# Kernel tuning notes

Measured on AMD Instinct MI355X. Metric: run time of the kernel, lower is better.

Reference implementation:

```python
import jax, jax.numpy as jnp
import numpy as np

N_ITER = 5  # Newton-Schulz iterations (matches n_iter default in source)


def _isqrt_newton_schulz_batch(A, num_iters):
    # A: [B, C, C] SPD matrices -> A^{-1/2} via coupled Newton-Schulz,
    # exactly mirroring isqrt_newton_schulz_autograd_batch in the source.
    b, dim, _ = A.shape
    normA = jnp.sqrt(jnp.sum(A * A, axis=(1, 2), keepdims=True))  # Frobenius norm per batch
    Y = A / normA
    I = jnp.broadcast_to(jnp.eye(dim, dtype=A.dtype), A.shape)
    Z = I
    for _ in range(num_iters):
        T = 0.5 * (3.0 * I - Z @ Y)
        Y = Y @ T
        Z = T @ Z
    return Z / jnp.sqrt(normA)


def setup_inputs() -> dict:
    key = jax.random.key(0)
    k1, k2, k3 = jax.random.split(key, 3)
    B, C, H, W = 8, 256, 128, 128
    r = 8  # reduction
    x = jax.random.normal(k1, (B, C, H, W), dtype=jnp.float32)
    w1 = jax.random.normal(k2, (C // r, C), dtype=jnp.float32) * 0.05  # squeeze 1x1 conv
    b1 = jnp.zeros((C // r,), dtype=jnp.float32)
    w2 = jax.random.normal(k3, (C, C // r), dtype=jnp.float32) * 0.05  # excite 1x1 conv
    b2 = jnp.zeros((C,), dtype=jnp.float32)
    return {"x": x, "w1": w1, "b1": b1, "w2": w2, "b2": b2}


def reference(x, w1, b1, w2, b2):
    B, C, H, W = x.shape
    M = H * W
    # global second-order (covariance) pooling
    xf = x.reshape(B, C, M)
    xc = xf - jnp.mean(xf, axis=-1, keepdims=True)          # center over spatial dim
    cov = jnp.einsum('bcm,bdm->bcd', xc, xc) / M            # [B, C, C]
    A_isqrt = _isqrt_newton_schulz_batch(cov, N_ITER)       # [B, C, C]
    # channel statistic: row mean of the matrix-(inverse-)sqrt
    y = jnp.mean(A_isqrt, axis=-1)                          # [B, C]
    # squeeze-excite gating (1x1 convs == dense over channels)
    h = jax.nn.relu(y @ w1.T + b1)                          # [B, C//r]
    g = jax.nn.sigmoid(h @ w2.T + b2)                       # [B, C]
    return x * g[:, :, None, None]
```

## Files before the change

### kernel.cpp

```cpp
#include <hip/hip_runtime.h>
#include <cstdint>
#include <cstddef>

typedef short s8vec __attribute__((ext_vector_type(8)));
typedef float f16acc __attribute__((ext_vector_type(16)));

#define C_DIM 256
#define M_DIM 16384
#define BATCH 8
#define KSPLIT 32
#define KCHUNK 512
#define BK 64
#define LDSP 72

static __device__ __forceinline__ unsigned short f2bf(float f) {
    union { float f; unsigned u; } v; v.f = f;
    unsigned r = v.u + 0x7fffu + ((v.u >> 16) & 1u);
    return (unsigned short)(r >> 16);
}
static __device__ __forceinline__ float bf2f(unsigned short h) {
    union { unsigned u; float f; } v; v.u = ((unsigned)h) << 16;
    return v.f;
}

__global__ __launch_bounds__(1024, 1)
void cov_kernel(const float* __restrict__ x, float* __restrict__ covraw,
                float* __restrict__ sums)
{
    __shared__ unsigned short Xs[C_DIM][LDSP];
    const int b   = blockIdx.y;
    const int kc  = blockIdx.x;
    const int tid = threadIdx.x;
    const int lane = tid & 63;
    const int wave = tid >> 6;
    const int wr = wave >> 2;
    const int wc = wave & 3;
    const int half = lane >> 5;
    const int l31  = lane & 31;

    const float* xb = x + (size_t)b * C_DIM * M_DIM + (size_t)kc * KCHUNK;

    f16acc acc[2][2] = {};
    float rowsum[4] = {0, 0, 0, 0};
    const int r0 = tid >> 4;
    const int c0 = (tid & 15) * 4;

    float4 v[4];
    {
        const float* src = xb + (size_t)r0 * M_DIM + c0;
        #pragma unroll
        for (int i = 0; i < 4; ++i)
            v[i] = *(const float4*)(src + (size_t)(64 * i) * M_DIM);
    }

    for (int kt = 0; kt < KCHUNK / BK; ++kt) {
        __syncthreads();
        #pragma unroll
        for (int i = 0; i < 4; ++i) {
            rowsum[i] += v[i].x + v[i].y + v[i].z + v[i].w;
            ushort4 p;
            p.x = f2bf(v[i].x); p.y = f2bf(v[i].y);
            p.z = f2bf(v[i].z); p.w = f2bf(v[i].w);
            *(ushort4*)&Xs[r0 + 64 * i][c0] = p;
        }
        if (kt < KCHUNK / BK - 1) {
            const float* src = xb + (size_t)r0 * M_DIM + (kt + 1) * BK + c0;
            #pragma unroll
            for (int i = 0; i < 4; ++i)
                v[i] = *(const float4*)(src + (size_t)(64 * i) * M_DIM);
        }
        __syncthreads();
        #pragma unroll
        for (int ks = 0; ks < 4; ++ks) {
            const int k0 = ks * 16 + half * 8;
            s8vec af[2], bfr[2];
            #pragma unroll
            for (int i = 0; i < 2; ++i)
                af[i] = *(const s8vec*)&Xs[wr * 64 + i * 32 + l31][k0];
            #pragma unroll
            for (int j = 0; j < 2; ++j)
                bfr[j] = *(const s8vec*)&Xs[wc * 64 + j * 32 + l31][k0];
            #pragma unroll
            for (int i = 0; i < 2; ++i)
                #pragma unroll
                for (int j = 0; j < 2; ++j)
                    acc[i][j] = __builtin_amdgcn_mfma_f32_32x32x16_bf16(
                        af[i], bfr[j], acc[i][j], 0, 0, 0);
        }
    }
    #pragma unroll
    for (int i = 0; i < 4; ++i) {
        float s = rowsum[i];
        s += __shfl_down(s, 8, 16);
        s += __shfl_down(s, 4, 16);
        s += __shfl_down(s, 2, 16);
        s += __shfl_down(s, 1, 16);
        if ((lane & 15) == 0)
            atomicAdd(&sums[b * C_DIM + r0 + 64 * i], s);
    }
    float* covb = covraw + (size_t)b * C_DIM * C_DIM;
    #pragma unroll
    for (int i = 0; i < 2; ++i) {
        const int rb = wr * 64 + i * 32 + 4 * half;
        #pragma unroll
        for (int j = 0; j < 2; ++j) {
            const int cb = wc * 64 + j * 32 + l31;
            #pragma unroll
            for (int r = 0; r < 16; ++r) {
                const int row = rb + (r & 3) + 8 * (r >> 2);
                atomicAdd(&covb[row * C_DIM + cb], acc[i][j][r]);
            }
        }
    }
}

__global__ __launch_bounds__(1024)
void finalize_cov(const float* __restrict__ covraw, const float* __restrict__ sums,
                  float* __restrict__ normA_g, unsigned short* __restrict__ Y0,
                  unsigned short* __restrict__ T0)
{
    const int b = blockIdx.x;
    const int tid = threadIdx.x;
    const float invM = 1.0f / (float)M_DIM;
    const float* cb = covraw + (size_t)b * 65536;
    const float* sb = sums + b * 256;
    float ss = 0.0f;
    #pragma unroll 4
    for (int i = 0; i < 64; ++i) {
        const int e = tid + i * 1024;
        const int r = e >> 8, c = e & 255;
        float v = cb[e] * invM - (sb[r] * invM) * (sb[c] * invM);
        ss += v * v;
    }
    __shared__ float red[16];
    __shared__ float sh_inv;
    float s = ss;
    #pragma unroll
    for (int off = 32; off; off >>= 1) s += __shfl_down(s, off, 64);
    if ((tid & 63) == 0) red[tid >> 6] = s;
    __syncthreads();
    if (tid == 0) {
        float t = 0.0f;
        #pragma unroll
        for (int i = 0; i < 16; ++i) t += red[i];
        float na = sqrtf(t);
        normA_g[b] = na;
        sh_inv = 1.0f / na;
    }
    __syncthreads();
    const float inv = sh_inv;
    unsigned short* yb = Y0 + (size_t)b * 65536;
    unsigned short* tb = T0 + (size_t)b * 65536;
    #pragma unroll 4
    for (int i = 0; i < 64; ++i) {
        const int e = tid + i * 1024;
        const int r = e >> 8, c = e & 255;
        float v = (cb[e] * invM - (sb[r] * invM) * (sb[c] * invM)) * inv;
        yb[e] = f2bf(v);
        tb[e] = f2bf(((r == c) ? 1.5f : 0.0f) - 0.5f * v);
    }
}

__global__ __launch_bounds__(256, 4)
void ns_stage(const unsigned short* __restrict__ A0, const unsigned short* __restrict__ B0,
              unsigned short* __restrict__ C0,
              const unsigned short* __restrict__ A1, const unsigned short* __restrict__ B1,
              unsigned short* __restrict__ C1,
              float c0, float c1)
{
    __shared__ unsigned short As[64][LDSP];
    __shared__ unsigned short Bs[64][LDSP];
    const int b = blockIdx.y;
    const int trow = (blockIdx.x >> 2) * 64, tcol = (blockIdx.x & 3) * 64;
    const unsigned short* A = (blockIdx.z ? A1 : A0) + (size_t)b * 65536;
    const unsigned short* B = (blockIdx.z ? B1 : B0) + (size_t)b * 65536;
    unsigned short* Cp = (blockIdx.z ? C1 : C0) + (size_t)b * 65536;

    const int tid = threadIdx.x;
    const int lane = tid & 63, wave = tid >> 6;
    const int wr = wave >> 1, wc = wave & 1;
    const int half = lane >> 5, l31 = lane & 31;

    f16acc acc = {};

    const int sr = tid >> 3;
    const int sc = (tid & 7) * 8;
    for (int kt = 0; kt < 4; ++kt) {
        const int kb = kt * BK;
        uint4 va[2], vb[2];
        #pragma unroll
        for (int i = 0; i < 2; ++i) {
            va[i] = *(const uint4*)(A + (size_t)(trow + sr + 32 * i) * 256 + kb + sc);
            vb[i] = *(const uint4*)(B + (size_t)(tcol + sr + 32 * i) * 256 + kb + sc);
        }
        __syncthreads();
        #pragma unroll
        for (int i = 0; i < 2; ++i) {
            *(uint4*)&As[sr + 32 * i][sc] = va[i];
            *(uint4*)&Bs[sr + 32 * i][sc] = vb[i];
        }
        __syncthreads();
        #pragma unroll
        for (int ks = 0; ks < 4; ++ks) {
            const int k0 = ks * 16 + half * 8;
            s8vec af = *(const s8vec*)&As[wr * 32 + l31][k0];
            s8vec bfr = *(const s8vec*)&Bs[wc * 32 + l31][k0];
            acc = __builtin_amdgcn_mfma_f32_32x32x16_bf16(af, bfr, acc, 0, 0, 0);
        }
    }
    const int rb = trow + wr * 32 + 4 * half;
    const int cb = tcol + wc * 32 + l31;
    #pragma unroll
    for (int r = 0; r < 16; ++r) {
        const int row = rb + (r & 3) + 8 * (r >> 2);
        float v = c1 * acc[r] + ((row == cb) ? c0 : 0.0f);
        Cp[row * 256 + cb] = f2bf(v);
    }
}

__global__ __launch_bounds__(256)
void gating_kernel(const unsigned short* __restrict__ Zfin, const float* __restrict__ normA_g,
                   const float* __restrict__ w1, const float* __restrict__ b1,
                   const float* __restrict__ w2, const float* __restrict__ b2,
                   float* __restrict__ g)
{
    const int b = blockIdx.x;
    const int tid = threadIdx.x;
    __shared__ float sy[256];
    __shared__ float sh[32];
    const unsigned short* zr = Zfin + (size_t)b * 65536 + (size_t)tid * 256;
    float s = 0.0f;
    #pragma unroll
    for (int i = 0; i < 32; ++i) {
        uint4 v = *(const uint4*)(zr + i * 8);
        const unsigned short* p = (const unsigned short*)&v;
        #pragma unroll
        for (int j = 0; j < 8; ++j) s += bf2f(p[j]);
    }
    const float scale = (1.0f / 256.0f) / sqrtf(normA_g[b]);
    sy[tid] = s * scale;
    __syncthreads();
    if (tid < 32) {
        float hh = b1[tid];
        const float* w1r = w1 + tid * 256;
        for (int c = 0; c < 256; ++c) hh += w1r[c] * sy[c];
        sh[tid] = hh > 0.0f ? hh : 0.0f;
    }
    __syncthreads();
    float z = b2[tid];
    const float* w2r = w2 + tid * 32;
    #pragma unroll
    for (int j = 0; j < 32; ++j) z += w2r[j] * sh[j];
    g[b * 256 + tid] = 1.0f / (1.0f + expf(-z));
}

__global__ __launch_bounds__(256)
void scale_kernel(const float* __restrict__ x, const float* __restrict__ g,
                  float* __restrict__ out)
{
    const float4* x4 = (const float4*)x;
    float4* o4 = (float4*)out;
    #pragma unroll
    for (int it = 0; it < 4; ++it) {
        size_t i = (size_t)blockIdx.x * 1024 + it * 256 + threadIdx.x;
        float gg = g[i >> 12];
        float4 v = x4[i];
        float4 r;
        r.x = v.x * gg; r.y = v.y * gg; r.z = v.z * gg; r.w = v.w * gg;
        o4[i] = r;
    }
}

extern "C" void kernel_launch(void* const* d_in, const int* in_sizes, int n_in,
                              void* d_out, int out_size, void* d_ws, size_t ws_size,
                              hipStream_t stream)
{
    const float* x  = (const float*)d_in[0];
    const float* w1 = (const float*)d_in[1];
    const float* b1 = (const float*)d_in[2];
    const float* w2 = (const float*)d_in[3];
    const float* b2 = (const float*)d_in[4];
    float* out = (float*)d_out;

    char* ws = (char*)d_ws;
    float* covraw = (float*)ws;
    float* sums   = (float*)(ws + 2097152);
    float* normA  = (float*)(ws + 2105344);
    float* g      = (float*)(ws + 2106368);
    unsigned short* Ya = (unsigned short*)(ws + 4194304);
    unsigned short* Yb = (unsigned short*)(ws + 5242880);
    unsigned short* Za = (unsigned short*)(ws + 6291456);
    unsigned short* Zb = (unsigned short*)(ws + 7340032);
    unsigned short* T  = (unsigned short*)(ws + 8388608);

    hipMemsetAsync(covraw, 0, 2105344, stream);

    cov_kernel<<<dim3(KSPLIT, BATCH), 1024, 0, stream>>>(x, covraw, sums);
    finalize_cov<<<BATCH, 1024, 0, stream>>>(covraw, sums, normA, Ya, Za);

    ns_stage<<<dim3(16, BATCH, 1), 256, 0, stream>>>(Ya, Za, Yb, Ya, Za, Yb, 0.0f, 1.0f);

    unsigned short* Ycur = Yb; unsigned short* Yoth = Ya;
    unsigned short* Zcur = Za; unsigned short* Zoth = Zb;
    for (int it = 0; it < 4; ++it) {
        ns_stage<<<dim3(16, BATCH, 1), 256, 0, stream>>>(
            Zcur, Ycur, T, Zcur, Ycur, T, 1.5f, -0.5f);
        if (it < 3) {
            ns_stage<<<dim3(16, BATCH, 2), 256, 0, stream>>>(
                Ycur, T, Yoth, T, Zcur, Zoth, 0.0f, 1.0f);
            unsigned short* t0 = Ycur; Ycur = Yoth; Yoth = t0;
            unsigned short* t1 = Zcur; Zcur = Zoth; Zoth = t1;
        } else {
            ns_stage<<<dim3(16, BATCH, 1), 256, 0, stream>>>(
                T, Zcur, Zoth, T, Zcur, Zoth, 0.0f, 1.0f);
            Zcur = Zoth;
        }
    }
    gating_kernel<<<BATCH, 256, 0, stream>>>(Zcur, normA, w1, b1, w2, b2, g);
    scale_kernel<<<8192, 256, 0, stream>>>(x, g, out);
}
```

Measured before the change: 447.7 us.

## Exploit covariance symmetry in split-K cov kernel and parallelize finalize

```diff
diff --git a/kernel.cpp b/kernel.cpp
--- a/kernel.cpp
+++ b/kernel.cpp
@@ -23,51 +23,78 @@
     return v.f;
 }
 
-__global__ __launch_bounds__(1024, 1)
+__global__ __launch_bounds__(256, 2)
 void cov_kernel(const float* __restrict__ x, float* __restrict__ covraw,
                 float* __restrict__ sums)
 {
-    __shared__ unsigned short Xs[C_DIM][LDSP];
-    const int b   = blockIdx.y;
-    const int kc  = blockIdx.x;
-    const int tid = threadIdx.x;
+    __shared__ unsigned short As[128][LDSP];
+    __shared__ unsigned short Bs[128][LDSP];
+    const int tile = blockIdx.x;
+    const int kc   = blockIdx.y;
+    const int b    = blockIdx.z;
+    const int trow = (tile == 0) ? 0 : 128;
+    const int tcol = (tile == 2) ? 0 : trow;
+    const bool diag = (tile < 2);
+
+    const int tid  = threadIdx.x;
     const int lane = tid & 63;
     const int wave = tid >> 6;
-    const int wr = wave >> 2;
-    const int wc = wave & 3;
-    const int half = lane >> 5;
-    const int l31  = lane & 31;
+    const int wr = wave >> 1, wc = wave & 1;
+    const int half = lane >> 5, l31 = lane & 31;
 
     const float* xb = x + (size_t)b * C_DIM * M_DIM + (size_t)kc * KCHUNK;
 
     f16acc acc[2][2] = {};
-    float rowsum[4] = {0, 0, 0, 0};
-    const int r0 = tid >> 4;
-    const int c0 = (tid & 15) * 4;
-
-    float4 v[4];
+    float rowsum[8] = {0,0,0,0,0,0,0,0};
+    const int sr = tid >> 4;
+    const int sc = (tid & 15) * 4;
+
+    float4 va[8], vb[8];
     {
-        const float* src = xb + (size_t)r0 * M_DIM + c0;
-        #pragma unroll
-        for (int i = 0; i < 4; ++i)
-            v[i] = *(const float4*)(src + (size_t)(64 * i) * M_DIM);
-    }
+        const float* sa = xb + (size_t)(trow + sr) * M_DIM + sc;
+        #pragma unroll
+        for (int i = 0; i < 8; ++i)
+            va[i] = *(const float4*)(sa + (size_t)(16 * i) * M_DIM);
+        if (!diag) {
+            const float* sb2 = xb + (size_t)(tcol + sr) * M_DIM + sc;
+            #pragma unroll
+            for (int i = 0; i < 8; ++i)
+                vb[i] = *(const float4*)(sb2 + (size_t)(16 * i) * M_DIM);
+        }
+    }
+
+    const unsigned short (*Bp)[LDSP] = diag ? As : Bs;
 
     for (int kt = 0; kt < KCHUNK / BK; ++kt) {
         __syncthreads();
         #pragma unroll
-        for (int i = 0; i < 4; ++i) {
-            rowsum[i] += v[i].x + v[i].y + v[i].z + v[i].w;
+        for (int i = 0; i < 8; ++i) {
+            if (diag) rowsum[i] += va[i].x + va[i].y + va[i].z + va[i].w;
             ushort4 p;
-            p.x = f2bf(v[i].x); p.y = f2bf(v[i].y);
-            p.z = f2bf(v[i].z); p.w = f2bf(v[i].w);
-            *(ushort4*)&Xs[r0 + 64 * i][c0] = p;
+            p.x = f2bf(va[i].x); p.y = f2bf(va[i].y);
+            p.z = f2bf(va[i].z); p.w = f2bf(va[i].w);
+            *(ushort4*)&As[sr + 16 * i][sc] = p;
+        }
+        if (!diag) {
+            #pragma unroll
+            for (int i = 0; i < 8; ++i) {
+                ushort4 p;
+                p.x = f2bf(vb[i].x); p.y = f2bf(vb[i].y);
+                p.z = f2bf(vb[i].z); p.w = f2bf(vb[i].w);
+                *(ushort4*)&Bs[sr + 16 * i][sc] = p;
+            }
         }
         if (kt < KCHUNK / BK - 1) {
-            const float* src = xb + (size_t)r0 * M_DIM + (kt + 1) * BK + c0;
-            #pragma unroll
-            for (int i = 0; i < 4; ++i)
-                v[i] = *(const float4*)(src + (size_t)(64 * i) * M_DIM);
+            const float* sa = xb + (size_t)(trow + sr) * M_DIM + (kt + 1) * BK + sc;
+            #pragma unroll
+            for (int i = 0; i < 8; ++i)
+                va[i] = *(const float4*)(sa + (size_t)(16 * i) * M_DIM);
+            if (!diag) {
+                const float* sb2 = xb + (size_t)(tcol + sr) * M_DIM + (kt + 1) * BK + sc;
+                #pragma unroll
+                for (int i = 0; i < 8; ++i)
+                    vb[i] = *(const float4*)(sb2 + (size_t)(16 * i) * M_DIM);
+            }
         }
         __syncthreads();
         #pragma unroll
@@ -76,10 +103,10 @@
             s8vec af[2], bfr[2];
             #pragma unroll
             for (int i = 0; i < 2; ++i)
-                af[i] = *(const s8vec*)&Xs[wr * 64 + i * 32 + l31][k0];
+                af[i] = *(const s8vec*)&As[wr * 64 + i * 32 + l31][k0];
             #pragma unroll
             for (int j = 0; j < 2; ++j)
-                bfr[j] = *(const s8vec*)&Xs[wc * 64 + j * 32 + l31][k0];
+                bfr[j] = *(const s8vec*)&Bp[wc * 64 + j * 32 + l31][k0];
             #pragma unroll
             for (int i = 0; i < 2; ++i)
                 #pragma unroll
@@ -88,23 +115,25 @@
                         af[i], bfr[j], acc[i][j], 0, 0, 0);
         }
     }
-    #pragma unroll
-    for (int i = 0; i < 4; ++i) {
-        float s = rowsum[i];
-        s += __shfl_down(s, 8, 16);
-        s += __shfl_down(s, 4, 16);
-        s += __shfl_down(s, 2, 16);
-        s += __shfl_down(s, 1, 16);
-        if ((lane & 15) == 0)
-            atomicAdd(&sums[b * C_DIM + r0 + 64 * i], s);
+    if (diag) {
+        #pragma unroll
+        for (int i = 0; i < 8; ++i) {
+            float s = rowsum[i];
+            s += __shfl_down(s, 8, 16);
+            s += __shfl_down(s, 4, 16);
+            s += __shfl_down(s, 2, 16);
+            s += __shfl_down(s, 1, 16);
+            if ((lane & 15) == 0)
+                atomicAdd(&sums[b * C_DIM + trow + sr + 16 * i], s);
+        }
     }
     float* covb = covraw + (size_t)b * C_DIM * C_DIM;
     #pragma unroll
     for (int i = 0; i < 2; ++i) {
-        const int rb = wr * 64 + i * 32 + 4 * half;
+        const int rb = trow + wr * 64 + i * 32 + 4 * half;
         #pragma unroll
         for (int j = 0; j < 2; ++j) {
-            const int cb = wc * 64 + j * 32 + l31;
+            const int cb = tcol + wc * 64 + j * 32 + l31;
             #pragma unroll
             for (int r = 0; r < 16; ++r) {
                 const int row = rb + (r & 3) + 8 * (r >> 2);
@@ -114,48 +143,56 @@
     }
 }
 
-__global__ __launch_bounds__(1024)
-void finalize_cov(const float* __restrict__ covraw, const float* __restrict__ sums,
-                  float* __restrict__ normA_g, unsigned short* __restrict__ Y0,
-                  unsigned short* __restrict__ T0)
-{
-    const int b = blockIdx.x;
-    const int tid = threadIdx.x;
+__global__ __launch_bounds__(256)
+void cov_normsq(const float* __restrict__ covraw, const float* __restrict__ sums,
+                float* __restrict__ normsq)
+{
+    const int slab = blockIdx.x;
+    const int b    = blockIdx.y;
+    const int tid  = threadIdx.x;
     const float invM = 1.0f / (float)M_DIM;
     const float* cb = covraw + (size_t)b * 65536;
     const float* sb = sums + b * 256;
     float ss = 0.0f;
     #pragma unroll 4
-    for (int i = 0; i < 64; ++i) {
-        const int e = tid + i * 1024;
+    for (int i = 0; i < 32; ++i) {
+        const int e = slab * 8192 + i * 256 + tid;
         const int r = e >> 8, c = e & 255;
-        float v = cb[e] * invM - (sb[r] * invM) * (sb[c] * invM);
+        const float raw = (r < 128 && c >= 128) ? cb[c * 256 + r] : cb[e];
+        const float v = raw * invM - (sb[r] * invM) * (sb[c] * invM);
         ss += v * v;
     }
-    __shared__ float red[16];
-    __shared__ float sh_inv;
-    float s = ss;
-    #pragma unroll
-    for (int off = 32; off; off >>= 1) s += __shfl_down(s, off, 64);
-    if ((tid & 63) == 0) red[tid >> 6] = s;
+    #pragma unroll
+    for (int off = 32; off; off >>= 1) ss += __shfl_down(ss, off, 64);
+    __shared__ float red[4];
+    if ((tid & 63) == 0) red[tid >> 6] = ss;
     __syncthreads();
-    if (tid == 0) {
-        float t = 0.0f;
-        #pragma unroll
-        for (int i = 0; i < 16; ++i) t += red[i];
-        float na = sqrtf(t);
-        normA_g[b] = na;
-        sh_inv = 1.0f / na;
-    }
-    __syncthreads();
-    const float inv = sh_inv;
+    if (tid == 0)
+        atomicAdd(&normsq[b], red[0] + red[1] + red[2] + red[3]);
+}
+
+__global__ __launch_bounds__(256)
+void emit_YT(const float* __restrict__ covraw, const float* __restrict__ sums,
+             const float* __restrict__ normsq, float* __restrict__ normA_g,
+             unsigned short* __restrict__ Y0, unsigned short* __restrict__ T0)
+{
+    const int slab = blockIdx.x;
+    const int b    = blockIdx.y;
+    const int tid  = threadIdx.x;
+    const float invM = 1.0f / (float)M_DIM;
+    const float nq  = normsq[b];
+    const float inv = rsqrtf(nq);
+    if (slab == 0 && tid == 0) normA_g[b] = sqrtf(nq);
+    const float* cb = covraw + (size_t)b * 65536;
+    const float* sb = sums + b * 256;
     unsigned short* yb = Y0 + (size_t)b * 65536;
     unsigned short* tb = T0 + (size_t)b * 65536;
     #pragma unroll 4
-    for (int i = 0; i < 64; ++i) {
-        const int e = tid + i * 1024;
+    for (int i = 0; i < 32; ++i) {
+        const int e = slab * 8192 + i * 256 + tid;
         const int r = e >> 8, c = e & 255;
-        float v = (cb[e] * invM - (sb[r] * invM) * (sb[c] * invM)) * inv;
+        const float raw = (r < 128 && c >= 128) ? cb[c * 256 + r] : cb[e];
+        const float v = (raw * invM - (sb[r] * invM) * (sb[c] * invM)) * inv;
         yb[e] = f2bf(v);
         tb[e] = f2bf(((r == c) ? 1.5f : 0.0f) - 0.5f * v);
     }
@@ -285,7 +322,8 @@
     char* ws = (char*)d_ws;
     float* covraw = (float*)ws;
     float* sums   = (float*)(ws + 2097152);
-    float* normA  = (float*)(ws + 2105344);
+    float* normsq = (float*)(ws + 2105344);
+    float* normA  = (float*)(ws + 2105600);
     float* g      = (float*)(ws + 2106368);
     unsigned short* Ya = (unsigned short*)(ws + 4194304);
     unsigned short* Yb = (unsigned short*)(ws + 5242880);
@@ -293,10 +331,11 @@
     unsigned short* Zb = (unsigned short*)(ws + 7340032);
     unsigned short* T  = (unsigned short*)(ws + 8388608);
 
-    hipMemsetAsync(covraw, 0, 2105344, stream);
-
-    cov_kernel<<<dim3(KSPLIT, BATCH), 1024, 0, stream>>>(x, covraw, sums);
-    finalize_cov<<<BATCH, 1024, 0, stream>>>(covraw, sums, normA, Ya, Za);
+    hipMemsetAsync(covraw, 0, 2105408, stream);
+
+    cov_kernel<<<dim3(3, KSPLIT, BATCH), 256, 0, stream>>>(x, covraw, sums);
+    cov_normsq<<<dim3(8, BATCH), 256, 0, stream>>>(covraw, sums, normsq);
+    emit_YT<<<dim3(8, BATCH), 256, 0, stream>>>(covraw, sums, normsq, normA, Ya, Za);
 
     ns_stage<<<dim3(16, BATCH, 1), 256, 0, stream>>>(Ya, Za, Yb, Ya, Za, Yb, 0.0f, 1.0f);
 
```

Result: faster. 388.1 us (-13.3%).
